# Performance work log

Hardware: AMD Instinct MI355X
Metric: run time of the kernel (lower is better)

## Reference

```python
import jax, jax.numpy as jnp
import numpy as np

V, D, L, H, FF, S = 32000, 400, 6, 8, 1600, 2048
B, N = 2, 2048
HD = D // H


def setup_inputs() -> dict:
    key = jax.random.key(0)
    ks = jax.random.split(key, 9)
    n = lambda k, shape: 0.02 * jax.random.normal(k, shape, dtype=jnp.float32)
    return {
        "idx": jax.random.randint(ks[0], (B, N), 0, V),
        "tok_emb": n(ks[1], (V, D)),
        "pos_emb": n(ks[2], (S, D)),
        "ln1_w": jnp.ones((L, D), jnp.float32), "ln1_b": jnp.zeros((L, D), jnp.float32),
        "qkv_w": n(ks[3], (L, D, 3 * D)), "qkv_b": jnp.zeros((L, 3 * D), jnp.float32),
        "attn_out_w": n(ks[4], (L, D, D)), "attn_out_b": jnp.zeros((L, D), jnp.float32),
        "ln2_w": jnp.ones((L, D), jnp.float32), "ln2_b": jnp.zeros((L, D), jnp.float32),
        "fc1_w": n(ks[5], (L, D, FF)), "fc1_b": jnp.zeros((L, FF), jnp.float32),
        "fc2_w": n(ks[6], (L, FF, D)), "fc2_b": jnp.zeros((L, D), jnp.float32),
        "lnf_w": jnp.ones((D,), jnp.float32), "lnf_b": jnp.zeros((D,), jnp.float32),
        "head_w": n(ks[7], (D, V)),
    }


def _ln(x, w, b):
    m = x.mean(-1, keepdims=True)
    v = ((x - m) ** 2).mean(-1, keepdims=True)
    return (x - m) * jax.lax.rsqrt(v + 1e-5) * w + b


def reference(idx, tok_emb, pos_emb, ln1_w, ln1_b, qkv_w, qkv_b, attn_out_w, attn_out_b,
              ln2_w, ln2_b, fc1_w, fc1_b, fc2_w, fc2_b, lnf_w, lnf_b, head_w):
    b, n = idx.shape
    scale = HD ** -0.5
    x = tok_emb[idx] + pos_emb[None, :n]          # [B,N,D]
    mask = jnp.tril(jnp.ones((n, n), dtype=bool))  # causal mask
    for l in range(L):
        h = _ln(x, ln1_w[l], ln1_b[l])
        qkv = h @ qkv_w[l] + qkv_b[l]
        q, k, v = jnp.split(qkv, 3, axis=-1)
        q = q.reshape(b, n, H, HD)
        k = k.reshape(b, n, H, HD)
        v = v.reshape(b, n, H, HD)
        s = jnp.einsum('bihd,bjhd->bhij', q, k) * scale   # [B,H,N,N]
        s = jnp.where(mask, s, -jnp.inf)
        a = jax.nn.softmax(s, axis=-1)
        o = jnp.einsum('bhij,bjhd->bihd', a, v).reshape(b, n, D)
        x = x + o @ attn_out_w[l] + attn_out_b[l]
        h = _ln(x, ln2_w[l], ln2_b[l])
        x = x + jax.nn.gelu(h @ fc1_w[l] + fc1_b[l], approximate=False) @ fc2_w[l] + fc2_b[l]
    return _ln(x, lnf_w, lnf_b) @ head_w          # [B,N,V] logits
```

## Files before the change

kernel.cpp:

```cpp
#include <hip/hip_runtime.h>
#include <hip/hip_bf16.h>
#include <math.h>

constexpr int V  = 32000;
constexpr int D  = 400;
constexpr int L  = 6;
constexpr int H  = 8;
constexpr int FF = 1600;
constexpr int B  = 2;
constexpr int N  = 2048;
constexpr int HD = D / H;
constexpr int TD = 3 * D;
constexpr int M  = B * N;
constexpr int KP = 416;

typedef __bf16 bf16x8 __attribute__((ext_vector_type(8)));
typedef float  f32x4  __attribute__((ext_vector_type(4)));
typedef unsigned short us16x4 __attribute__((ext_vector_type(4)));

static __device__ __forceinline__ float wave_sum_f(float v) {
#pragma unroll
    for (int m = 32; m; m >>= 1) v += __shfl_xor(v, m, 64);
    return v;
}

static __device__ __forceinline__ void gl_lds16(const unsigned short* g, unsigned short* l) {
    __builtin_amdgcn_global_load_lds(
        (const __attribute__((address_space(1))) unsigned int*)(g),
        (__attribute__((address_space(3))) unsigned int*)(l), 16, 0, 0);
}

static __device__ __forceinline__ unsigned short f2bf(float f) {
    __hip_bfloat16 h = __float2bfloat16(f);
    return *reinterpret_cast<unsigned short*>(&h);
}

__global__ __launch_bounds__(256) void embed_ln_kernel(const int* __restrict__ idx,
                                                       const float* __restrict__ tok,
                                                       const float* __restrict__ pos,
                                                       const float* __restrict__ lnw,
                                                       const float* __restrict__ lnb,
                                                       float* __restrict__ x,
                                                       __hip_bfloat16* __restrict__ hb) {
    const int row  = blockIdx.x * 4 + (threadIdx.x >> 6);
    const int lane = threadIdx.x & 63;
    const int n = row & (N - 1);
    const float* tr = tok + (size_t)idx[row] * D;
    const float* pr = pos + (size_t)n * D;

    float v[7];
    float s = 0.f, ss = 0.f;
#pragma unroll
    for (int i = 0; i < 7; ++i) {
        const int d = lane + i * 64;
        if (d < D) {
            v[i] = tr[d] + pr[d];
            s += v[i]; ss += v[i] * v[i];
        } else v[i] = 0.f;
    }
    s  = wave_sum_f(s);
    ss = wave_sum_f(ss);
    const float mean = s * (1.0f / D);
    const float var  = ss * (1.0f / D) - mean * mean;
    const float rstd = rsqrtf(var + 1e-5f);

    float* xr = x + (size_t)row * D;
    __hip_bfloat16* hr = hb + (size_t)row * KP;
#pragma unroll
    for (int i = 0; i < 7; ++i) {
        const int d = lane + i * 64;
        if (d < D) {
            xr[d] = v[i];
            hr[d] = __float2bfloat16((v[i] - mean) * rstd * lnw[d] + lnb[d]);
        } else if (d < KP) {
            hr[d] = __float2bfloat16(0.f);
        }
    }
}

__global__ __launch_bounds__(256) void ln_bf16_kernel(const float* __restrict__ in,
                                                      const float* __restrict__ w,
                                                      const float* __restrict__ b,
                                                      __hip_bfloat16* __restrict__ out) {
    const int row  = blockIdx.x * 4 + (threadIdx.x >> 6);
    const int lane = threadIdx.x & 63;
    const float* xr = in + (size_t)row * D;
    float s = 0.f, ss = 0.f;
    for (int d = lane; d < D; d += 64) {
        float v = xr[d];
        s += v; ss += v * v;
    }
    s  = wave_sum_f(s);
    ss = wave_sum_f(ss);
    float mean = s * (1.0f / D);
    float var  = ss * (1.0f / D) - mean * mean;
    float rstd = rsqrtf(var + 1e-5f);
    __hip_bfloat16* orow = out + (size_t)row * KP;
    for (int d = lane; d < KP; d += 64)
        orow[d] = __float2bfloat16(d < D ? (xr[d] - mean) * rstd * w[d] + b[d] : 0.f);
}

__global__ __launch_bounds__(256) void wconv_all_kernel(const float* __restrict__ qkv_w,
                                                        const float* __restrict__ ao_w,
                                                        const float* __restrict__ fc1_w,
                                                        const float* __restrict__ fc2_w,
                                                        __hip_bfloat16* __restrict__ qkvt,
                                                        __hip_bfloat16* __restrict__ aot,
                                                        __hip_bfloat16* __restrict__ fc1t,
                                                        __hip_bfloat16* __restrict__ fc2t) {
    const int bid = blockIdx.x;
    int t, rem;
    if      (bid < 3120) { t = 0; rem = bid; }
    else if (bid < 4368) { t = 1; rem = bid - 3120; }
    else if (bid < 8424) { t = 2; rem = bid - 4368; }
    else                 { t = 3; rem = bid - 8424; }
    const int  tilesPerL[4] = {520, 208, 676, 800};
    const int  nkt[4]  = {13, 13, 13, 50};
    const int  Ka[4]   = {400, 400, 400, 1600};
    const int  Nwa[4]  = {1200, 400, 1600, 400};
    const int  Kpa[4]  = {416, 416, 416, 1600};
    const int  Nra[4]  = {1280, 512, 1664, 512};
    const long sWa[4]  = {480000L, 160000L, 640000L, 640000L};
    const long sBta[4] = {532480L, 212992L, 692224L, 819200L};
    const float* W = t == 0 ? qkv_w : t == 1 ? ao_w : t == 2 ? fc1_w : fc2_w;
    __hip_bfloat16* Bt = t == 0 ? qkvt : t == 1 ? aot : t == 2 ? fc1t : fc2t;
    const int l = rem / tilesPerL[t];
    const int tile = rem % tilesPerL[t];
    const int k0 = (tile % nkt[t]) * 32, n0 = (tile / nkt[t]) * 32;
    const int K = Ka[t], Nw = Nwa[t], Kp = Kpa[t], Nr = Nra[t];

    __shared__ float tt[32][33];
    const float* Wl = W + (size_t)l * sWa[t];
    __hip_bfloat16* Btl = Bt + (size_t)l * sBta[t];
    for (int i = 0; i < 32; i += 8) {
        int k = k0 + threadIdx.y + i, n = n0 + threadIdx.x;
        tt[threadIdx.y + i][threadIdx.x] = (k < K && n < Nw) ? Wl[(size_t)k * Nw + n] : 0.f;
    }
    __syncthreads();
    for (int i = 0; i < 32; i += 8) {
        int n = n0 + threadIdx.y + i, k = k0 + threadIdx.x;
        if (n < Nr && k < Kp) Btl[(size_t)n * Kp + k] = __float2bfloat16(tt[threadIdx.x][threadIdx.y + i]);
    }
}

__global__ __launch_bounds__(256) void wconv_kernel(const float* __restrict__ W,
                                                    __hip_bfloat16* __restrict__ Bt,
                                                    int K, int Nw, int Kp, int Nr) {
    __shared__ float t[32][33];
    const int k0 = blockIdx.x * 32, n0 = blockIdx.y * 32;
    for (int i = 0; i < 32; i += 8) {
        int k = k0 + threadIdx.y + i, n = n0 + threadIdx.x;
        t[threadIdx.y + i][threadIdx.x] = (k < K && n < Nw) ? W[(size_t)k * Nw + n] : 0.f;
    }
    __syncthreads();
    for (int i = 0; i < 32; i += 8) {
        int n = n0 + threadIdx.y + i, k = k0 + threadIdx.x;
        if (n < Nr && k < Kp) Bt[(size_t)n * Kp + k] = __float2bfloat16(t[threadIdx.x][threadIdx.y + i]);
    }
}

__global__ __launch_bounds__(256) void mmwide_kernel(const unsigned short* __restrict__ A,
                                                     const unsigned short* __restrict__ Bt,
                                                     float* __restrict__ C,
                                                     int Nc, int Kp) {
    __shared__ __align__(1024) unsigned short As[128 * 32];
    __shared__ __align__(1024) unsigned short Bs[256 * 32];
    const int tid  = threadIdx.x;
    const int lane = tid & 63, wid = tid >> 6;
    const int wr = wid >> 1, wc = wid & 1;
    const int l15 = lane & 15, g = lane >> 4;

    const int nwg  = gridDim.x * gridDim.y;
    const int cpx  = nwg >> 3;
    const int f    = blockIdx.y * gridDim.x + blockIdx.x;
    const int swz  = (f & 7) * cpx + (f >> 3);
    const int by   = swz & (gridDim.x - 1);
    const int bx   = swz >> 5;

    f32x4 acc[4][8] = {};

    const unsigned short* Abase = A  + (size_t)(by * 128) * Kp;
    const unsigned short* Bbase = Bt + (size_t)(bx * 256) * Kp;
    const int lrow = lane >> 2;
    const int lcol = (lane & 3) * 8;

    for (int k0 = 0; k0 < Kp; k0 += 32) {
#pragma unroll
        for (int c = 0; c < 2; ++c) {
            const int chunk = wid * 2 + c;
            gl_lds16(Abase + (size_t)(chunk * 16 + lrow) * Kp + k0 + lcol, As + chunk * 512);
        }
#pragma unroll
        for (int c = 0; c < 4; ++c) {
            const int chunk = wid * 4 + c;
            gl_lds16(Bbase + (size_t)(chunk * 16 + lrow) * Kp + k0 + lcol, Bs + chunk * 512);
        }
        __syncthreads();
        bf16x8 a[4], b[8];
#pragma unroll
        for (int m = 0; m < 4; ++m)
            a[m] = *(const bf16x8*)(As + (wr * 64 + m * 16 + l15) * 32 + g * 8);
#pragma unroll
        for (int n = 0; n < 8; ++n)
            b[n] = *(const bf16x8*)(Bs + (wc * 128 + n * 16 + l15) * 32 + g * 8);
#pragma unroll
        for (int m = 0; m < 4; ++m)
#pragma unroll
            for (int n = 0; n < 8; ++n)
                acc[m][n] = __builtin_amdgcn_mfma_f32_16x16x32_bf16(a[m], b[n], acc[m][n], 0, 0, 0);
        __syncthreads();
    }

    const int col_base = bx * 256 + wc * 128 + l15;
    const int row_base = by * 128 + wr * 64 + (g << 2);
#pragma unroll
    for (int n = 0; n < 8; ++n) {
        const int col = col_base + n * 16;
        if (col >= Nc) continue;
#pragma unroll
        for (int m = 0; m < 4; ++m) {
#pragma unroll
            for (int r = 0; r < 4; ++r) {
                const int row = row_base + m * 16 + r;
                C[(size_t)row * Nc + col] = acc[m][n][r];
            }
        }
    }
}

template <bool BIAS, bool RES, bool GELU, bool OUTBF>
__global__ __launch_bounds__(256) void mm64_kernel(const unsigned short* __restrict__ A,
                                                   const unsigned short* __restrict__ Bt,
                                                   const float* __restrict__ bias,
                                                   const float* __restrict__ res,
                                                   void* __restrict__ Cv,
                                                   int Nc, int Kp) {
    __shared__ __align__(1024) unsigned short As[64 * 32];
    __shared__ __align__(1024) unsigned short Bs[128 * 32];
    const int tid  = threadIdx.x;
    const int lane = tid & 63, wid = tid >> 6;
    const int wr = wid >> 1, wc = wid & 1;
    const int bx = blockIdx.x, by = blockIdx.y;
    const int l15 = lane & 15, g = lane >> 4;

    f32x4 acc[2][4] = {};

    const unsigned short* Abase = A  + (size_t)(by * 64) * Kp;
    const unsigned short* Bbase = Bt + (size_t)(bx * 128) * Kp;
    const int lrow = lane >> 2;
    const int lcol = (lane & 3) * 8;

    for (int k0 = 0; k0 < Kp; k0 += 32) {
        gl_lds16(Abase + (size_t)(wid * 16 + lrow) * Kp + k0 + lcol, As + wid * 512);
#pragma unroll
        for (int c = 0; c < 2; ++c) {
            const int chunk = wid * 2 + c;
            gl_lds16(Bbase + (size_t)(chunk * 16 + lrow) * Kp + k0 + lcol, Bs + chunk * 512);
        }
        __syncthreads();
        bf16x8 a[2], b[4];
#pragma unroll
        for (int m = 0; m < 2; ++m)
            a[m] = *(const bf16x8*)(As + (wr * 32 + m * 16 + l15) * 32 + g * 8);
#pragma unroll
        for (int n = 0; n < 4; ++n)
            b[n] = *(const bf16x8*)(Bs + (wc * 64 + n * 16 + l15) * 32 + g * 8);
#pragma unroll
        for (int m = 0; m < 2; ++m)
#pragma unroll
            for (int n = 0; n < 4; ++n)
                acc[m][n] = __builtin_amdgcn_mfma_f32_16x16x32_bf16(a[m], b[n], acc[m][n], 0, 0, 0);
        __syncthreads();
    }

    const int col_base = bx * 128 + wc * 64 + l15;
    const int row_base = by * 64 + wr * 32 + (g << 2);
#pragma unroll
    for (int n = 0; n < 4; ++n) {
        const int col = col_base + n * 16;
        if (col >= Nc) continue;
        const float bv = BIAS ? bias[col] : 0.f;
#pragma unroll
        for (int m = 0; m < 2; ++m) {
#pragma unroll
            for (int r = 0; r < 4; ++r) {
                const int row = row_base + m * 16 + r;
                float v = acc[m][n][r] + bv;
                if (GELU) v = 0.5f * v * (1.0f + erff(v * 0.70710678118654752f));
                const size_t ci = (size_t)row * Nc + col;
                if (RES) v += res[ci];
                if (OUTBF) ((__hip_bfloat16*)Cv)[ci] = __float2bfloat16(v);
                else       ((float*)Cv)[ci] = v;
            }
        }
    }
}

__global__ __launch_bounds__(256) void mm_qkv_kernel(const unsigned short* __restrict__ A,
                                                     const unsigned short* __restrict__ Bt,
                                                     const float* __restrict__ bias,
                                                     unsigned short* __restrict__ Qb,
                                                     unsigned short* __restrict__ Kb,
                                                     unsigned short* __restrict__ Vt) {
    __shared__ __align__(1024) unsigned short As[128 * 32];
    __shared__ __align__(1024) unsigned short Bs[128 * 32];
    const int tid  = threadIdx.x;
    const int lane = tid & 63, wid = tid >> 6;
    const int wr = wid >> 1, wc = wid & 1;
    const int bx = blockIdx.x, by = blockIdx.y;

    f32x4 acc[4][4] = {};

    const unsigned short* Abase = A  + (size_t)(by * 128) * KP;
    const unsigned short* Bbase = Bt + (size_t)(bx * 128) * KP;
    const int lrow = lane >> 2;
    const int lcol = (lane & 3) * 8;

    for (int k0 = 0; k0 < KP; k0 += 32) {
#pragma unroll
        for (int c = 0; c < 2; ++c) {
            const int chunk = wid * 2 + c;
            gl_lds16(Abase + (size_t)(chunk * 16 + lrow) * KP + k0 + lcol, As + chunk * 512);
            gl_lds16(Bbase + (size_t)(chunk * 16 + lrow) * KP + k0 + lcol, Bs + chunk * 512);
        }
        __syncthreads();
        bf16x8 a[4], b[4];
#pragma unroll
        for (int m = 0; m < 4; ++m)
            a[m] = *(const bf16x8*)(As + (wr * 64 + m * 16 + (lane & 15)) * 32 + (lane >> 4) * 8);
#pragma unroll
        for (int n = 0; n < 4; ++n)
            b[n] = *(const bf16x8*)(Bs + (wc * 64 + n * 16 + (lane & 15)) * 32 + (lane >> 4) * 8);
#pragma unroll
        for (int m = 0; m < 4; ++m)
#pragma unroll
            for (int n = 0; n < 4; ++n)
                acc[m][n] = __builtin_amdgcn_mfma_f32_16x16x32_bf16(a[m], b[n], acc[m][n], 0, 0, 0);
        __syncthreads();
    }

    const float scale = 0.14142135623730950f;
    const int col_base = bx * 128 + wc * 64 + (lane & 15);
    const int row_base = by * 128 + wr * 64 + ((lane >> 4) << 2);
#pragma unroll
    for (int n = 0; n < 4; ++n) {
        const int col = col_base + n * 16;
        if (col >= TD) continue;
        const int part = col < D ? 0 : (col < 2 * D ? 1 : 2);
        const int cc = col - part * D;
        const int h = cc / HD, d = cc % HD;
        const float bv = bias[col];
#pragma unroll
        for (int m = 0; m < 4; ++m) {
            const int row0 = row_base + m * 16;
            const int b = row0 >> 11, nn0 = row0 & (N - 1);
            const int bh = b * H + h;
            if (part == 2) {
                us16x4 pk;
#pragma unroll
                for (int r = 0; r < 4; ++r) pk[r] = f2bf(acc[m][n][r] + bv);
                *(us16x4*)(Vt + (size_t)(bh * 64 + d) * N + nn0) = pk;
            } else if (part == 0) {
#pragma unroll
                for (int r = 0; r < 4; ++r)
                    Qb[(size_t)(bh * N + nn0 + r) * 64 + d] = f2bf((acc[m][n][r] + bv) * scale);
            } else {
#pragma unroll
                for (int r = 0; r < 4; ++r)
                    Kb[(size_t)(bh * N + nn0 + r) * 64 + d] = f2bf(acc[m][n][r] + bv);
            }
        }
    }
}

__global__ __launch_bounds__(256) void fattn_kernel(const unsigned short* __restrict__ Qb,
                                                    const unsigned short* __restrict__ Kb,
                                                    const unsigned short* __restrict__ Vt,
                                                    __hip_bfloat16* __restrict__ o) {
    const int q0 = blockIdx.x * 64, h = blockIdx.y, b = blockIdx.z;
    const int bh = b * H + h;
    const int tid = threadIdx.x, lane = tid & 63, w = tid >> 6;
    const int l15 = lane & 15, g = lane >> 4;

    __shared__ __align__(1024) unsigned short Ks[2][64 * 64];
    __shared__ __align__(1024) unsigned short Vs[2][64 * 64];
    __shared__ __hip_bfloat16 P_s[4][16 * 72];
    unsigned short* Pw = (unsigned short*)&P_s[w][0];

    const int st_r    = (lane >> 3);
    const int st_cblk = (lane ^ (lane >> 3)) & 7;

    const unsigned short* Qrow = Qb + ((size_t)(bh * N + q0 + w * 16 + l15)) * 64 + g * 8;
    const bf16x8 qa0 = *(const bf16x8*)(Qrow);
    const bf16x8 qa1 = *(const bf16x8*)(Qrow + 32);

    f32x4 acc[4] = {};
    float ssum[4] = {0.f, 0.f, 0.f, 0.f};

    const int nt = q0 / 64 + 1;

#define STAGE(buf, j0)                                                                     \
    {                                                                                      \
        _Pragma("unroll")                                                                  \
        for (int c = 0; c < 2; ++c) {                                                      \
            const int rr = (w * 2 + c) * 8 + st_r;                                         \
            gl_lds16(Kb + (size_t)(bh * N + (j0) + rr) * 64 + st_cblk * 8,                 \
                     &Ks[buf][(w * 2 + c) * 512]);                                         \
            gl_lds16(Vt + (size_t)(bh * 64 + rr) * N + (j0) + st_cblk * 8,                 \
                     &Vs[buf][(w * 2 + c) * 512]);                                         \
        }                                                                                  \
    }

    STAGE(0, 0);
    __syncthreads();

    for (int t = 0; t < nt; ++t) {
        const int cur = t & 1;
        if (t + 1 < nt) STAGE(cur ^ 1, (t + 1) * 64);

        f32x4 s[4];
        const int swz = ((l15 & 7) << 3);
#pragma unroll
        for (int n = 0; n < 4; ++n) {
            const unsigned short* kbase = &Ks[cur][(n * 16 + l15) * 64];
            bf16x8 k0 = *(const bf16x8*)(kbase + ((g * 8) ^ swz));
            bf16x8 k1 = *(const bf16x8*)(kbase + (((g + 4) * 8) ^ swz));
            f32x4 z = {};
            z    = __builtin_amdgcn_mfma_f32_16x16x32_bf16(qa0, k0, z, 0, 0, 0);
            s[n] = __builtin_amdgcn_mfma_f32_16x16x32_bf16(qa1, k1, z, 0, 0, 0);
        }
        if (t == nt - 1) {
#pragma unroll
            for (int n = 0; n < 4; ++n)
#pragma unroll
                for (int r = 0; r < 4; ++r)
                    if (l15 + n * 16 > w * 16 + g * 4 + r) s[n][r] = -INFINITY;
        }
#pragma unroll
        for (int n = 0; n < 4; ++n)
#pragma unroll
            for (int r = 0; r < 4; ++r) {
                float p = __expf(s[n][r]);
                ssum[r] += p;
                Pw[(g * 4 + r) * 72 + l15 + n * 16] = f2bf(p);
            }
        bf16x8 pa0 = *(const bf16x8*)(Pw + l15 * 72 + g * 8);
        bf16x8 pa1 = *(const bf16x8*)(Pw + l15 * 72 + 32 + g * 8);

#pragma unroll
        for (int n = 0; n < 4; ++n) {
            const unsigned short* vbase = &Vs[cur][(n * 16 + l15) * 64];
            bf16x8 v0 = *(const bf16x8*)(vbase + ((g * 8) ^ swz));
            bf16x8 v1 = *(const bf16x8*)(vbase + (((g + 4) * 8) ^ swz));
            acc[n] = __builtin_amdgcn_mfma_f32_16x16x32_bf16(pa0, v0, acc[n], 0, 0, 0);
            acc[n] = __builtin_amdgcn_mfma_f32_16x16x32_bf16(pa1, v1, acc[n], 0, 0, 0);
        }

        __syncthreads();
    }
#undef STAGE

#pragma unroll
    for (int r = 0; r < 4; ++r)
#pragma unroll
        for (int msk = 1; msk < 16; msk <<= 1) ssum[r] += __shfl_xor(ssum[r], msk, 64);

#pragma unroll
    for (int n = 0; n < 4; ++n) {
        const int d = n * 16 + l15;
        if (d < HD) {
#pragma unroll
            for (int r = 0; r < 4; ++r) {
                const int row = b * N + q0 + w * 16 + g * 4 + r;
                o[(size_t)row * KP + h * HD + d] = __float2bfloat16(acc[n][r] / ssum[r]);
            }
        }
    }
}

extern "C" void kernel_launch(void* const* d_in, const int* in_sizes, int n_in,
                              void* d_out, int out_size, void* d_ws, size_t ws_size,
                              hipStream_t stream) {
    const int*   idx        = (const int*)d_in[0];
    const float* tok_emb    = (const float*)d_in[1];
    const float* pos_emb    = (const float*)d_in[2];
    const float* ln1_w      = (const float*)d_in[3];
    const float* ln1_b      = (const float*)d_in[4];
    const float* qkv_w      = (const float*)d_in[5];
    const float* qkv_b      = (const float*)d_in[6];
    const float* attn_out_w = (const float*)d_in[7];
    const float* attn_out_b = (const float*)d_in[8];
    const float* ln2_w      = (const float*)d_in[9];
    const float* ln2_b      = (const float*)d_in[10];
    const float* fc1_w      = (const float*)d_in[11];
    const float* fc1_b      = (const float*)d_in[12];
    const float* fc2_w      = (const float*)d_in[13];
    const float* fc2_b      = (const float*)d_in[14];
    const float* lnf_w      = (const float*)d_in[15];
    const float* lnf_b      = (const float*)d_in[16];
    const float* head_w     = (const float*)d_in[17];
    float* out = (float*)d_out;

    char* ws = (char*)d_ws;
    __hip_bfloat16* hb   = (__hip_bfloat16*)(ws);
    float*          x    = (float*)(ws + 3407872);
    __hip_bfloat16* ff   = (__hip_bfloat16*)(ws + 9961472);
    __hip_bfloat16* ob   = (__hip_bfloat16*)(ws + 23068672);
    __hip_bfloat16* headt = (__hip_bfloat16*)(ws + 3407872);

    char* wout = (char*)d_out;
    __hip_bfloat16* qkvt = (__hip_bfloat16*)(wout);
    __hip_bfloat16* aot  = (__hip_bfloat16*)(wout + 6389760);
    __hip_bfloat16* fc1t = (__hip_bfloat16*)(wout + 8945664);
    __hip_bfloat16* fc2t = (__hip_bfloat16*)(wout + 17252352);
    unsigned short* qb_g = (unsigned short*)(wout + 27082752);
    unsigned short* kb_g = (unsigned short*)(wout + 31277056);
    unsigned short* vt_g = (unsigned short*)(wout + 35471360);

    wconv_all_kernel<<<dim3(13224), dim3(32, 8), 0, stream>>>(
        qkv_w, attn_out_w, fc1_w, fc2_w, qkvt, aot, fc1t, fc2t);

    embed_ln_kernel<<<dim3(M / 4), dim3(256), 0, stream>>>(idx, tok_emb, pos_emb, ln1_w, ln1_b, x, hb);
    hipMemsetAsync(ob, 0, (size_t)M * KP * sizeof(__hip_bfloat16), stream);
    hipMemsetAsync(qb_g, 0, 3 * 4194304, stream);

    for (int l = 0; l < L; ++l) {
        mm_qkv_kernel<<<dim3(10, 32), dim3(256), 0, stream>>>(
            (const unsigned short*)hb, (const unsigned short*)(qkvt + (size_t)l * 1280 * KP),
            qkv_b + (size_t)l * TD, qb_g, kb_g, vt_g);
        fattn_kernel<<<dim3(N / 64, H, B), dim3(256), 0, stream>>>(qb_g, kb_g, vt_g, ob);
        mm64_kernel<true, true, false, false><<<dim3(4, 64), dim3(256), 0, stream>>>(
            (const unsigned short*)ob, (const unsigned short*)(aot + (size_t)l * 512 * KP),
            attn_out_b + (size_t)l * D, x, x, D, KP);
        ln_bf16_kernel<<<dim3(M / 4), dim3(256), 0, stream>>>(x, ln2_w + (size_t)l * D, ln2_b + (size_t)l * D, hb);
        mm64_kernel<true, false, true, true><<<dim3(13, 64), dim3(256), 0, stream>>>(
            (const unsigned short*)hb, (const unsigned short*)(fc1t + (size_t)l * 1664 * KP),
            fc1_b + (size_t)l * FF, nullptr, ff, FF, KP);
        mm64_kernel<true, true, false, false><<<dim3(4, 64), dim3(256), 0, stream>>>(
            (const unsigned short*)ff, (const unsigned short*)(fc2t + (size_t)l * 512 * FF),
            fc2_b + (size_t)l * D, x, x, D, FF);
        const float* nw = (l < L - 1) ? ln1_w + (size_t)(l + 1) * D : lnf_w;
        const float* nb = (l < L - 1) ? ln1_b + (size_t)(l + 1) * D : lnf_b;
        ln_bf16_kernel<<<dim3(M / 4), dim3(256), 0, stream>>>(x, nw, nb, hb);
    }

    wconv_kernel<<<dim3(13, 1000), dim3(32, 8), 0, stream>>>(head_w, headt, D, V, KP, V);
    mmwide_kernel<<<dim3(32, 125), dim3(256), 0, stream>>>(
        (const unsigned short*)hb, (const unsigned short*)headt, out, V, KP);
}
```

Baseline: 1.141 ms.

## Restructure head GEMM to keep full-K A tile resident in LDS

Replaces the generic wide GEMM for the vocab head with a kernel that loads a 64-row by full-K activation tile into padded LDS once. It then loops over five 256-column output panels, reading B directly from global memory without LDS staging or per-k barriers. Output is written with nontemporal stores so the large logits array does not pollute the cache. This trades B reuse across rows (each block now covers only 64 rows, so B traffic doubles) for fewer syncs and less LDS staging. B loads are uncoalesced, strided row reads that may stall the MFMAs.

New measurement: 1.116 ms (median of 2 runs). 1.02x faster.

```diff
diff --git a/kernel.cpp b/kernel.cpp
--- a/kernel.cpp
+++ b/kernel.cpp
@@ -159,71 +159,58 @@
     }
 }
 
-__global__ __launch_bounds__(256) void mmwide_kernel(const unsigned short* __restrict__ A,
+__global__ __launch_bounds__(256) void mmhead_kernel(const unsigned short* __restrict__ A,
                                                      const unsigned short* __restrict__ Bt,
-                                                     float* __restrict__ C,
-                                                     int Nc, int Kp) {
-    __shared__ __align__(1024) unsigned short As[128 * 32];
-    __shared__ __align__(1024) unsigned short Bs[256 * 32];
-    const int tid  = threadIdx.x;
-    const int lane = tid & 63, wid = tid >> 6;
+                                                     float* __restrict__ C) {
+    __shared__ __align__(1024) unsigned short As[64 * 424];
+    const int tid = threadIdx.x, lane = tid & 63, wid = tid >> 6;
     const int wr = wid >> 1, wc = wid & 1;
     const int l15 = lane & 15, g = lane >> 4;
 
-    const int nwg  = gridDim.x * gridDim.y;
-    const int cpx  = nwg >> 3;
-    const int f    = blockIdx.y * gridDim.x + blockIdx.x;
-    const int swz  = (f & 7) * cpx + (f >> 3);
-    const int by   = swz & (gridDim.x - 1);
-    const int bx   = swz >> 5;
-
-    f32x4 acc[4][8] = {};
-
-    const unsigned short* Abase = A  + (size_t)(by * 128) * Kp;
-    const unsigned short* Bbase = Bt + (size_t)(bx * 256) * Kp;
-    const int lrow = lane >> 2;
-    const int lcol = (lane & 3) * 8;
-
-    for (int k0 = 0; k0 < Kp; k0 += 32) {
-#pragma unroll
-        for (int c = 0; c < 2; ++c) {
-            const int chunk = wid * 2 + c;
-            gl_lds16(Abase + (size_t)(chunk * 16 + lrow) * Kp + k0 + lcol, As + chunk * 512);
-        }
-#pragma unroll
-        for (int c = 0; c < 4; ++c) {
-            const int chunk = wid * 4 + c;
-            gl_lds16(Bbase + (size_t)(chunk * 16 + lrow) * Kp + k0 + lcol, Bs + chunk * 512);
-        }
-        __syncthreads();
-        bf16x8 a[4], b[8];
-#pragma unroll
-        for (int m = 0; m < 4; ++m)
-            a[m] = *(const bf16x8*)(As + (wr * 64 + m * 16 + l15) * 32 + g * 8);
-#pragma unroll
-        for (int n = 0; n < 8; ++n)
-            b[n] = *(const bf16x8*)(Bs + (wc * 128 + n * 16 + l15) * 32 + g * 8);
-#pragma unroll
-        for (int m = 0; m < 4; ++m)
+    const int f   = blockIdx.y * 64 + blockIdx.x;
+    const int swz = (f & 7) * 200 + (f >> 3);
+    const int by  = swz & 63;
+    const int pg  = swz >> 6;
+
+    const unsigned short* Ab = A + (size_t)(by * 64) * KP;
+    for (int i = tid; i < 64 * 52; i += 256) {
+        const int r = i / 52, c = (i % 52) * 8;
+        *(bf16x8*)(As + r * 424 + c) = *(const bf16x8*)(Ab + (size_t)r * KP + c);
+    }
+    __syncthreads();
+
+    const unsigned short* A0 = As + (wr * 32 + l15) * 424 + g * 8;
+    const unsigned short* A1 = A0 + 16 * 424;
+
+#pragma unroll
+    for (int p = 0; p < 5; ++p) {
+        const int col0 = (pg * 5 + p) * 256 + wc * 128;
+        const unsigned short* Bc = Bt + (size_t)col0 * KP + g * 8;
+        f32x4 acc[2][8] = {};
+#pragma unroll
+        for (int ks = 0; ks < 13; ++ks) {
+            const int k0 = ks * 32;
+            bf16x8 b[8];
 #pragma unroll
             for (int n = 0; n < 8; ++n)
-                acc[m][n] = __builtin_amdgcn_mfma_f32_16x16x32_bf16(a[m], b[n], acc[m][n], 0, 0, 0);
-        __syncthreads();
-    }
-
-    const int col_base = bx * 256 + wc * 128 + l15;
-    const int row_base = by * 128 + wr * 64 + (g << 2);
-#pragma unroll
-    for (int n = 0; n < 8; ++n) {
-        const int col = col_base + n * 16;
-        if (col >= Nc) continue;
-#pragma unroll
-        for (int m = 0; m < 4; ++m) {
-#pragma unroll
-            for (int r = 0; r < 4; ++r) {
-                const int row = row_base + m * 16 + r;
-                C[(size_t)row * Nc + col] = acc[m][n][r];
+                b[n] = *(const bf16x8*)(Bc + (size_t)(n * 16 + l15) * KP + k0);
+            const bf16x8 a0 = *(const bf16x8*)(A0 + k0);
+            const bf16x8 a1 = *(const bf16x8*)(A1 + k0);
+#pragma unroll
+            for (int n = 0; n < 8; ++n) {
+                acc[0][n] = __builtin_amdgcn_mfma_f32_16x16x32_bf16(a0, b[n], acc[0][n], 0, 0, 0);
+                acc[1][n] = __builtin_amdgcn_mfma_f32_16x16x32_bf16(a1, b[n], acc[1][n], 0, 0, 0);
             }
+        }
+        const int rowb = by * 64 + wr * 32 + (g << 2);
+#pragma unroll
+        for (int n = 0; n < 8; ++n) {
+            const int col = col0 + n * 16 + l15;
+#pragma unroll
+            for (int m = 0; m < 2; ++m)
+#pragma unroll
+                for (int r = 0; r < 4; ++r)
+                    __builtin_nontemporal_store(acc[m][n][r], &C[(size_t)(rowb + m * 16 + r) * V + col]);
         }
     }
 }
@@ -545,6 +532,6 @@
     }
 
     wconv_kernel<<<dim3(13, 1000), dim3(32, 8), 0, stream>>>(head_w, headt, D, V, KP, V);
-    mmwide_kernel<<<dim3(32, 125), dim3(256), 0, stream>>>(
-        (const unsigned short*)hb, (const unsigned short*)headt, out, V, KP);
-}
+    mmhead_kernel<<<dim3(64, 25), dim3(256), 0, stream>>>(
+        (const unsigned short*)hb, (const unsigned short*)headt, out);
+}
```
